# Kernel optimization log

Hardware: AMD Instinct MI355X
Metric: run time of the kernel (lower is better)

The kernel has to match this reference:

```python
import jax, jax.numpy as jnp
import numpy as np

E, B, S, C, N, D, DFF, H, K_FREQ = 4, 16, 256, 17, 16, 32, 64, 4, 4
DH = D // H
MA_KERNELS = (4, 8, 12)


def setup_inputs() -> dict:
    key = jax.random.key(0)
    ks = jax.random.split(key, 16)
    sc = 1.0 / np.sqrt(D).astype(np.float32)
    inp = {
        "x": jax.random.normal(ks[0], (B, S, C, 1), jnp.float32),
        "original_x": jax.random.uniform(ks[1], (B, S, 2), jnp.float32),
        "start_W": jax.random.normal(ks[2], (D,), jnp.float32),
        "start_b": jnp.zeros((D,), jnp.float32),
        "Wq": jax.random.normal(ks[3], (E, D, D), jnp.float32) * sc,
        "Wk": jax.random.normal(ks[4], (E, D, D), jnp.float32) * sc,
        "Wv": jax.random.normal(ks[5], (E, D, D), jnp.float32) * sc,
        "Wo": jax.random.normal(ks[6], (E, D, D), jnp.float32) * sc,
        "ln1_g": jnp.ones((E, D), jnp.float32),
        "ln1_b": jnp.zeros((E, D), jnp.float32),
        "ln2_g": jnp.ones((E, D), jnp.float32),
        "ln2_b": jnp.zeros((E, D), jnp.float32),
        "W1": jax.random.normal(ks[7], (E, D, DFF), jnp.float32) * sc,
        "b1": jnp.zeros((E, DFF), jnp.float32),
        "W2": jax.random.normal(ks[8], (E, DFF, D), jnp.float32) * (1.0 / np.sqrt(DFF).astype(np.float32)),
        "b2": jnp.zeros((E, D), jnp.float32),
    }
    return inp


def _moving_avg(x, k):
    # x: [B,S,Ch], replicate-pad then uniform window of size k (stride 1)
    front = jnp.repeat(x[:, :1], (k - 1) // 2, axis=1)
    end = jnp.repeat(x[:, -1:], k // 2, axis=1)
    xp = jnp.concatenate([front, x, end], axis=1)  # [B, S+k-1, Ch]
    c = jnp.cumsum(xp, axis=1)
    c = jnp.concatenate([jnp.zeros_like(c[:, :1]), c], axis=1)
    return (c[:, k:] - c[:, :-k]) / jnp.asarray(k, x.dtype)


def _fourier_season(x, k):
    # ETSformer-style FourierLayer: keep top-k amplitude frequencies (excluding DC)
    s = x.shape[1]
    xf = jnp.fft.rfft(x, axis=1)            # [B,F,Ch] complex
    amp = jnp.abs(xf)
    amp = amp.at[:, 0, :].set(-jnp.inf)     # exclude DC
    topv = jax.lax.top_k(jnp.moveaxis(amp, 1, -1), k)[0]  # [B,Ch,k]
    thresh = topv[..., -1]                  # [B,Ch]
    mask = amp >= thresh[:, None, :]
    xf_m = jnp.where(mask, xf, 0)
    return jnp.fft.irfft(xf_m, n=s, axis=1).astype(x.dtype)


def _ln(z, g, b):
    m = jnp.mean(z, -1, keepdims=True)
    v = jnp.var(z, -1, keepdims=True)
    return (z - m) * jax.lax.rsqrt(v + 1e-5) * g + b


def _expert_fwd(args):
    h, wq, wk, wv, wo, g1, bg1, g2, bg2, w1, b1e, w2, b2e = args
    # h: [B,S,N,D]; pre-LN MHA over the sequence axis per (batch, node)
    z = _ln(h, g1, bg1)
    q = jnp.einsum('bsnd,de->bsne', z, wq).reshape(B, S, N, H, DH)
    k_ = jnp.einsum('bsnd,de->bsne', z, wk).reshape(B, S, N, H, DH)
    v_ = jnp.einsum('bsnd,de->bsne', z, wv).reshape(B, S, N, H, DH)
    att = jnp.einsum('bqnhd,bknhd->bnhqk', q, k_) * (1.0 / np.sqrt(DH).astype(np.float32))
    att = jax.nn.softmax(att, axis=-1)
    o = jnp.einsum('bnhqk,bknhd->bqnhd', att, v_).reshape(B, S, N, D)
    h = h + jnp.einsum('bsnd,de->bsne', o, wo)
    z2 = _ln(h, g2, bg2)
    f = jax.nn.relu(jnp.einsum('bsnd,df->bsnf', z2, w1) + b1e)
    h = h + jnp.einsum('bsnf,fd->bsnd', f, w2) + b2e
    return h


def reference(x, original_x, start_W, start_b, Wq, Wk, Wv, Wo,
              ln1_g, ln1_b, ln2_g, ln2_b, W1, b1, W2, b2):
    xc = x[:, :, :, 0]                                  # [B,S,C]
    trend = sum(_moving_avg(xc, k) for k in MA_KERNELS) / float(len(MA_KERNELS))
    season = _fourier_season(xc, K_FREQ)
    new_x = xc + season + trend                         # [B,S,C]

    scores = original_x[:, :, -1]                       # [B,S]
    bins = jnp.linspace(scores.min(), scores.max(), E + 1)
    assign = jnp.clip(jnp.searchsorted(bins, scores, side='right') - 1, 0, E - 1)  # [B,S] int

    xns = new_x[:, :, :-1]                              # [B,S,N] drop score channel
    onehot = (assign[None] == jnp.arange(E)[:, None, None])          # [E,B,S] bool
    expert_in = xns[None] * onehot[..., None].astype(xns.dtype)      # [E,B,S,N] dense zero-padded dispatch
    hidden = expert_in[..., None] * start_W + start_b                # [E,B,S,N,D] start_linear

    outs = jax.lax.map(_expert_fwd, (hidden, Wq, Wk, Wv, Wo,
                                     ln1_g, ln1_b, ln2_g, ln2_b, W1, b1, W2, b2))  # [E,B,S,N,D]
    combined = jnp.einsum('ebs,ebsnd->bsnd', onehot.astype(outs.dtype), outs)      # one-hot combine
    return combined
```

## Files before the change

### kernel.cpp

```cpp
#include <hip/hip_runtime.h>
#include <math.h>

#define BB 16
#define SS 256
#define CC 17
#define NCH 16
#define DD 32
#define DFFN 64
#define HH 4
#define DH 8
#define EE 4

#define WS_K0 16
#define WS_V0 144
#define WS_XNS 512
#define WS_SPI (WS_XNS + BB*SS*NCH)
#define WS_WT  (WS_SPI + BB*SS + 64)
#define WS_WL  (WS_WT + 6144)

#define PRE 0.51006977f

typedef __fp16 hv2 __attribute__((ext_vector_type(2)));

__device__ __forceinline__ unsigned pkh2(float a, float b) {
  hv2 r = __builtin_amdgcn_cvt_pkrtz(a, b);
  unsigned u; __builtin_memcpy(&u, &r, 4);
  return u;
}
__device__ __forceinline__ float fd2(unsigned a, unsigned b, float c) {
  hv2 av, bv;
  __builtin_memcpy(&av, &a, 4);
  __builtin_memcpy(&bv, &b, 4);
  return __builtin_amdgcn_fdot2(av, bv, c, false);
}
__device__ __forceinline__ float h2lo(unsigned u) {
  hv2 v; __builtin_memcpy(&v, &u, 4); return (float)v[0];
}
__device__ __forceinline__ float h2hi(unsigned u) {
  hv2 v; __builtin_memcpy(&v, &u, 4); return (float)v[1];
}

__launch_bounds__(1024)
__global__ void decomp_prep_kernel(const float* __restrict__ x,
                                   const float* __restrict__ ox,
                                   const float* __restrict__ sb,
                                   const float* __restrict__ g1,
                                   const float* __restrict__ bb1,
                                   const float* __restrict__ Wq,
                                   const float* __restrict__ Wk,
                                   const float* __restrict__ Wv,
                                   const float* __restrict__ Wo,
                                   const float* __restrict__ W1,
                                   const float* __restrict__ W2,
                                   float* __restrict__ ws) {
  const int t = threadIdx.x;
  if (blockIdx.x < 256) {
    const int b = blockIdx.x / NCH;
    const int c = blockIdx.x % NCH;
    __shared__ float xs[SS];
    __shared__ float prr[1024], pii[1024];
    __shared__ float amp[129];
    __shared__ float2 YY[129];
    __shared__ float sth;
    if (t < SS) xs[t] = x[(b*SS + t)*CC + c];
    __syncthreads();
    const float TH0 = 0.024543692606170259f;
    {
      const int f = (t & 127) + 1;
      const int chunk = t >> 7;
      const int s0 = chunk * 32;
      const int ph0 = (f * s0) & 255;
      float si, cr; sincosf(TH0*(float)ph0, &si, &cr);
      float s1, c1; sincosf(TH0*(float)f, &s1, &c1);
      float xr = 0.f, xi = 0.f;
      #pragma unroll 4
      for (int k = 0; k < 32; ++k) {
        float xvv = xs[s0 + k];
        xr += xvv * cr;
        xi -= xvv * si;
        float nc = cr*c1 - si*s1;
        si = si*c1 + cr*s1;
        cr = nc;
      }
      prr[t] = xr; pii[t] = xi;
    }
    __syncthreads();
    if (t < 128) {
      float xr = 0.f, xi = 0.f;
      #pragma unroll
      for (int k2 = 0; k2 < 8; ++k2) { xr += prr[t + 128*k2]; xi += pii[t + 128*k2]; }
      prr[t] = xr; pii[t] = xi;
      amp[t+1] = sqrtf(xr*xr + xi*xi);
    }
    __syncthreads();
    if (t < 64) {
      float a0 = amp[t+1], a1 = amp[t+65];
      int i0 = t+1, i1 = t+65;
      float th = -1e30f;
      for (int r = 0; r < 4; ++r) {
        float mv = (a0 > a1) ? a0 : a1;
        int   mi = (a0 > a1) ? i0 : i1;
        for (int off = 32; off > 0; off >>= 1) {
          float ov = __shfl_xor(mv, off);
          int   oi = __shfl_xor(mi, off);
          if (ov > mv || (ov == mv && oi < mi)) { mv = ov; mi = oi; }
        }
        th = mv;
        if (mi == i0) a0 = -1e30f;
        if (mi == i1) a1 = -1e30f;
      }
      if (t == 0) sth = th;
    }
    __syncthreads();
    if (t < 128) {
      const int f = t + 1;
      float wgt = (amp[f] >= sth) ? ((f == 128) ? 1.0f : 2.0f) * (1.0f/256.0f) : 0.0f;
      YY[f] = make_float2(wgt * prr[t], wgt * pii[t]);
    }
    __syncthreads();
    {
      const int s = t & 255;
      const int fc = t >> 8;
      const int f0 = 1 + fc*32;
      const int ph0 = (s * f0) & 255;
      float si, cr; sincosf(TH0*(float)ph0, &si, &cr);
      float s1, c1; sincosf(TH0*(float)s, &s1, &c1);
      float acc = 0.f;
      #pragma unroll 4
      for (int k = 0; k < 32; ++k) {
        float2 y = YY[f0 + k];
        acc += y.x*cr - y.y*si;
        float nc = cr*c1 - si*s1;
        si = si*c1 + cr*s1;
        cr = nc;
      }
      prr[t] = acc;
    }
    __syncthreads();
    if (t < 256) {
      float season = prr[t] + prr[t+256] + prr[t+512] + prr[t+768];
      float s4 = 0.f, s8 = 0.f, s12 = 0.f;
      #pragma unroll
      for (int j = 0; j < 4; ++j)  { int p = t + j - 1; p = p < 0 ? 0 : (p > SS-1 ? SS-1 : p); s4  += xs[p]; }
      #pragma unroll
      for (int j = 0; j < 8; ++j)  { int p = t + j - 3; p = p < 0 ? 0 : (p > SS-1 ? SS-1 : p); s8  += xs[p]; }
      #pragma unroll
      for (int j = 0; j < 12; ++j) { int p = t + j - 5; p = p < 0 ? 0 : (p > SS-1 ? SS-1 : p); s12 += xs[p]; }
      float trend = (s4 * 0.25f + s8 * 0.125f + s12 * (1.0f/12.0f)) * (1.0f/3.0f);
      ws[WS_XNS + (b*SS + t)*NCH + c] = xs[t] + season + trend;
    }
  } else if (blockIdx.x < 272) {
    const int b = blockIdx.x - 256;
    __shared__ float red[32];
    __shared__ int asg[SS];
    __shared__ int cnt[EE];
    __shared__ float z0[EE*DD];
    float mn = 3e38f, mx = -3e38f;
    #pragma unroll
    for (int k = 0; k < 4; ++k) {
      float v = ox[(t + k*1024)*2 + 1];
      mn = fminf(mn, v); mx = fmaxf(mx, v);
    }
    for (int off = 32; off > 0; off >>= 1) {
      mn = fminf(mn, __shfl_xor(mn, off));
      mx = fmaxf(mx, __shfl_xor(mx, off));
    }
    if ((t & 63) == 0) { red[(t>>6)*2] = mn; red[(t>>6)*2+1] = mx; }
    __syncthreads();
    mn = red[0]; mx = red[1];
    #pragma unroll
    for (int w = 1; w < 16; ++w) { mn = fminf(mn, red[w*2]); mx = fmaxf(mx, red[w*2+1]); }
    const float step = (mx - mn) * 0.25f;
    const float e1 = mn + step, e2 = mn + 2.f*step, e3 = mn + 3.f*step;
    if (t < 256) {
      float sc = ox[(b*SS + t)*2 + 1];
      asg[t] = (sc >= e1) + (sc >= e2) + (sc >= e3);
    }
    __syncthreads();
    if (t < EE) {
      int c = 0;
      for (int s2 = 0; s2 < SS; ++s2) c += (asg[s2] == t);
      cnt[t] = c;
    }
    __syncthreads();
    int* SPw  = (int*)ws + WS_SPI;
    int* OFFw = SPw + BB*SS;
    if (t < EE) {
      int off = 0;
      for (int i = 0; i < t; ++i) off += cnt[i];
      OFFw[b*EE + t] = off;
      int kp = off;
      for (int s2 = 0; s2 < SS; ++s2) if (asg[s2] == t) SPw[b*SS + (kp++)] = s2;
    }
    if (t < 128) {
      int ee = t >> 5, d = t & 31;
      float m = 0.f;
      for (int i = 0; i < DD; ++i) m += sb[i];
      m *= (1.0f/DD);
      float var = 0.f;
      for (int i = 0; i < DD; ++i) { float df = sb[i]-m; var += df*df; }
      var *= (1.0f/DD);
      float rs = rsqrtf(var + 1e-5f);
      z0[ee*DD + d] = (sb[d]-m)*rs*g1[ee*DD+d] + bb1[ee*DD+d];
    }
    __syncthreads();
    if (b == 0 && t < 128) {
      int ee = t >> 5, d = t & 31;
      float k0 = 0.f, v0 = 0.f;
      for (int i = 0; i < DD; ++i) {
        float zz = z0[ee*DD + i];
        k0 += zz * Wk[ee*DD*DD + i*DD + d];
        v0 += zz * Wv[ee*DD*DD + i*DD + d];
      }
      ws[WS_K0 + ee*DD + d] = k0;
      ws[WS_V0 + ee*DD + d] = v0;
    }
  } else {
    unsigned* img = (unsigned*)ws + WS_WT;
    const int base_u = (blockIdx.x - 272)*4096;
    #pragma unroll
    for (int i = 0; i < 4; ++i) {
      int u = base_u + i*1024 + t;
      unsigned val;
      if (u < 6144) {
        int mat = u >> 11, r = u & 2047;
        int row = r >> 4, ip = r & 15;
        int e = row >> 5, q = row & 31;
        int d = (q & 3)*8 + (q >> 2);
        const float* Wm = (mat == 0) ? Wq : (mat == 1) ? Wk : Wv;
        const float* src = Wm + e*1024 + d;
        val = pkh2(src[ip*64], src[ip*64 + 32]);
      } else {
        int v = u - 6144;
        if (v < 2048) {
          int row = v >> 4, ip = v & 15;
          int e = row >> 5, q = row & 31;
          int d = (q & 3)*8 + (q >> 2);
          const float* src = Wo + e*1024 + d;
          val = pkh2(src[ip*64], src[ip*64 + 32]);
        } else if (v < 6144) {
          int r = v - 2048;
          int row = r >> 4, ip = r & 15;
          int e = row >> 6, q = row & 63;
          int j = (q & 3)*16 + (q >> 2);
          const float* src = W1 + e*2048 + j;
          val = pkh2(src[ip*128], src[ip*128 + 64]);
        } else {
          int r = v - 6144;
          int a = r >> 11, rr = r & 2047;
          int row = rr >> 4, ip = rr & 15;
          int e = row >> 5, q = row & 31;
          int d = (q & 3)*8 + (q >> 2);
          int jp = a*16 + ip;
          const float* src = W2 + e*2048 + d;
          val = pkh2(src[2*jp*32], src[(2*jp+1)*32]);
        }
      }
      img[u] = val;
    }
  }
}

__launch_bounds__(1024, 4)
__global__ void fused_kernel(const float* __restrict__ ws,
    const float* __restrict__ g1, const float* __restrict__ bb1,
    const float* __restrict__ sW, const float* __restrict__ sb,
    const float* __restrict__ g2, const float* __restrict__ bb2,
    const float* __restrict__ b1, const float* __restrict__ b2,
    float* __restrict__ out) {
  const int blk = blockIdx.x;
  const int n = blk & 15;
  const int b = blk >> 4;
  const int t = threadIdx.x;
  const int p = t >> 2;
  const int hh = t & 3;
  __shared__ unsigned lds[24576];
  float* fl = (float*)lds;
  unsigned* wT = lds + 8192;
  unsigned* wl = lds + 14336;

  {
    const uint4* simg = (const uint4*)((const unsigned*)ws + WS_WT);
    uint4* dst = (uint4*)wT;
    #pragma unroll
    for (int i = 0; i < 4; ++i) dst[i*1024 + t] = simg[i*1024 + t];
  }

  const int* SP  = (const int*)ws + WS_SPI;
  const int* OFF = SP + BB*SS;
  const int o1 = OFF[b*4+1], o2 = OFF[b*4+2], o3 = OFF[b*4+3];
  const int e = (p >= o1) + (p >= o2) + (p >= o3);
  const int beg = (e==0) ? 0  : ((e==1) ? o1 : ((e==2) ? o2 : o3));
  const int end = (e==0) ? o1 : ((e==1) ? o2 : ((e==2) ? o3 : SS));
  const int s = SP[b*SS + p];
  const float xv = ws[WS_XNS + (b*SS + s)*NCH + n];

  float h[DD];
  #pragma unroll
  for (int d = 0; d < DD; ++d) h[d] = xv * sW[d] + sb[d];
  float m = 0.f;
  #pragma unroll
  for (int d = 0; d < DD; ++d) m += h[d];
  m *= (1.0f/DD);
  float var = 0.f;
  #pragma unroll
  for (int d = 0; d < DD; ++d) { float df = h[d]-m; var += df*df; }
  var *= (1.0f/DD);
  float rs = rsqrtf(var + 1e-5f);
  unsigned zp[16];
  #pragma unroll
  for (int ip = 0; ip < 16; ++ip) {
    float za = (h[2*ip]  -m)*rs*g1[e*DD+2*ip]   + bb1[e*DD+2*ip];
    float zb = (h[2*ip+1]-m)*rs*g1[e*DD+2*ip+1] + bb1[e*DD+2*ip+1];
    zp[ip] = pkh2(za, zb);
  }
  __syncthreads();

  float q[DH], kk[DH], vv[DH];
  #pragma unroll
  for (int dd = 0; dd < DH; ++dd) {
    const int row16 = (e*32 + dd*4 + hh)*16;
    const uint4* rq = (const uint4*)&wT[row16];
    const uint4* rk = (const uint4*)&wT[2048 + row16];
    const uint4* rv = (const uint4*)&wT[4096 + row16];
    float aq = 0.f, ak = 0.f, av = 0.f;
    #pragma unroll
    for (int g4 = 0; g4 < 4; ++g4) {
      uint4 wq4 = rq[g4], wk4 = rk[g4], wv4 = rv[g4];
      aq = fd2(zp[4*g4+0], wq4.x, aq); aq = fd2(zp[4*g4+1], wq4.y, aq);
      aq = fd2(zp[4*g4+2], wq4.z, aq); aq = fd2(zp[4*g4+3], wq4.w, aq);
      ak = fd2(zp[4*g4+0], wk4.x, ak); ak = fd2(zp[4*g4+1], wk4.y, ak);
      ak = fd2(zp[4*g4+2], wk4.z, ak); ak = fd2(zp[4*g4+3], wk4.w, ak);
      av = fd2(zp[4*g4+0], wv4.x, av); av = fd2(zp[4*g4+1], wv4.y, av);
      av = fd2(zp[4*g4+2], wv4.z, av); av = fd2(zp[4*g4+3], wv4.w, av);
    }
    q[dd] = aq * PRE; kk[dd] = ak; vv[dd] = av;
  }
  *(uint4*)&lds[p*32 + hh*8]     = make_uint4(pkh2(kk[0],kk[1]), pkh2(kk[2],kk[3]),
                                              pkh2(kk[4],kk[5]), pkh2(kk[6],kk[7]));
  *(uint4*)&lds[p*32 + hh*8 + 4] = make_uint4(pkh2(vv[0],vv[1]), pkh2(vv[2],vv[3]),
                                              pkh2(vv[4],vv[5]), pkh2(vv[6],vv[7]));
  unsigned qp2[4];
  #pragma unroll
  for (int i = 0; i < 4; ++i) qp2[i] = pkh2(q[2*i], q[2*i+1]);
  float s0 = 0.f;
  #pragma unroll
  for (int d = 0; d < DH; ++d) s0 += q[d] * ws[WS_K0 + e*DD + hh*DH + d];
  float v0s[DH];
  #pragma unroll
  for (int d = 0; d < DH; ++d) v0s[d] = ws[WS_V0 + e*DD + hh*DH + d];
  __syncthreads();

  float wsum = 0.f;
  float o[DH] = {0,0,0,0,0,0,0,0};
  for (int jk = beg; jk < end; ++jk) {
    uint4 ku = *(const uint4*)&lds[jk*32 + hh*8];
    uint4 vu = *(const uint4*)&lds[jk*32 + hh*8 + 4];
    float a = 0.f;
    a = fd2(qp2[0], ku.x, a); a = fd2(qp2[1], ku.y, a);
    a = fd2(qp2[2], ku.z, a); a = fd2(qp2[3], ku.w, a);
    float w = __builtin_amdgcn_exp2f(a);
    wsum += w;
    o[0] += w*h2lo(vu.x); o[1] += w*h2hi(vu.x);
    o[2] += w*h2lo(vu.y); o[3] += w*h2hi(vu.y);
    o[4] += w*h2lo(vu.z); o[5] += w*h2hi(vu.z);
    o[6] += w*h2lo(vu.w); o[7] += w*h2hi(vu.w);
  }
  const int nmis = SS - (end - beg);
  float w0 = (float)nmis * __builtin_amdgcn_exp2f(s0);
  wsum += w0;
  #pragma unroll
  for (int d = 0; d < DH; ++d) o[d] += w0 * v0s[d];
  float inv = 1.0f / wsum;
  #pragma unroll
  for (int d = 0; d < DH; ++d) o[d] *= inv;
  __syncthreads();

  #pragma unroll
  for (int d = 0; d < DH; ++d) fl[p*33 + hh*DH + d] = o[d];
  __syncthreads();
  unsigned ovp[16];
  #pragma unroll
  for (int ip = 0; ip < 16; ++ip) ovp[ip] = pkh2(fl[p*33 + 2*ip], fl[p*33 + 2*ip+1]);

  float acc[DH];
  #pragma unroll
  for (int dd = 0; dd < DH; ++dd) {
    int d = hh*DH + dd;
    const uint4* row = (const uint4*)&wl[(e*32 + dd*4 + hh)*16];
    float a = xv * sW[d] + sb[d];
    #pragma unroll
    for (int g4 = 0; g4 < 4; ++g4) {
      uint4 w4 = row[g4];
      a = fd2(ovp[4*g4+0], w4.x, a); a = fd2(ovp[4*g4+1], w4.y, a);
      a = fd2(ovp[4*g4+2], w4.z, a); a = fd2(ovp[4*g4+3], w4.w, a);
    }
    acc[dd] = a;
  }
  __syncthreads();
  #pragma unroll
  for (int dd = 0; dd < DH; ++dd) fl[p*33 + hh*DH + dd] = acc[dd];
  __syncthreads();

  float h2r[DD];
  #pragma unroll
  for (int i = 0; i < DD; ++i) h2r[i] = fl[p*33 + i];
  m = 0.f;
  #pragma unroll
  for (int d = 0; d < DD; ++d) m += h2r[d];
  m *= (1.0f/DD);
  var = 0.f;
  #pragma unroll
  for (int d = 0; d < DD; ++d) { float df = h2r[d]-m; var += df*df; }
  var *= (1.0f/DD);
  rs = rsqrtf(var + 1e-5f);
  unsigned zp2[16];
  #pragma unroll
  for (int ip = 0; ip < 16; ++ip) {
    float za = (h2r[2*ip]  -m)*rs*g2[e*DD+2*ip]   + bb2[e*DD+2*ip];
    float zb = (h2r[2*ip+1]-m)*rs*g2[e*DD+2*ip+1] + bb2[e*DD+2*ip+1];
    zp2[ip] = pkh2(za, zb);
  }
  float hres[DH];
  #pragma unroll
  for (int dd = 0; dd < DH; ++dd) hres[dd] = h2r[hh*DH + dd];
  __syncthreads();

  float f[16];
  #pragma unroll
  for (int jj = 0; jj < 16; ++jj) {
    const uint4* row = (const uint4*)&wl[2048 + (e*64 + jj*4 + hh)*16];
    float a = b1[e*DFFN + hh*16 + jj];
    #pragma unroll
    for (int g4 = 0; g4 < 4; ++g4) {
      uint4 w4 = row[g4];
      a = fd2(zp2[4*g4+0], w4.x, a); a = fd2(zp2[4*g4+1], w4.y, a);
      a = fd2(zp2[4*g4+2], w4.z, a); a = fd2(zp2[4*g4+3], w4.w, a);
    }
    f[jj] = fmaxf(a, 0.0f);
  }
  {
    uint4 fa = make_uint4(pkh2(f[0],f[1]), pkh2(f[2],f[3]), pkh2(f[4],f[5]), pkh2(f[6],f[7]));
    uint4 fb = make_uint4(pkh2(f[8],f[9]), pkh2(f[10],f[11]), pkh2(f[12],f[13]), pkh2(f[14],f[15]));
    *(uint4*)&lds[p*36 + hh*8]     = fa;
    *(uint4*)&lds[p*36 + hh*8 + 4] = fb;
  }
  __syncthreads();

  uint4 fpr[8];
  #pragma unroll
  for (int g4 = 0; g4 < 8; ++g4) fpr[g4] = *(const uint4*)&lds[p*36 + 4*g4];
  float acc2[DH];
  #pragma unroll
  for (int dd = 0; dd < DH; ++dd) {
    int d = hh*DH + dd;
    const int row16 = (e*32 + dd*4 + hh)*16;
    float a = hres[dd] + b2[e*DD + d];
    #pragma unroll
    for (int g4 = 0; g4 < 8; ++g4) {
      const int plane = (g4 >> 2);
      uint4 w4 = *(const uint4*)&wl[6144 + plane*2048 + row16 + 4*(g4 & 3)];
      uint4 fq = fpr[g4];
      a = fd2(fq.x, w4.x, a); a = fd2(fq.y, w4.y, a);
      a = fd2(fq.z, w4.z, a); a = fd2(fq.w, w4.w, a);
    }
    acc2[dd] = a;
  }
  float* op = out + ((size_t)((b*SS + s)*NCH + n))*DD + hh*DH;
  *(float4*)(op)     = make_float4(acc2[0], acc2[1], acc2[2], acc2[3]);
  *(float4*)(op + 4) = make_float4(acc2[4], acc2[5], acc2[6], acc2[7]);
}

extern "C" void kernel_launch(void* const* d_in, const int* in_sizes, int n_in,
                              void* d_out, int out_size, void* d_ws, size_t ws_size,
                              hipStream_t stream) {
  (void)in_sizes; (void)n_in; (void)out_size; (void)ws_size;
  const float* x   = (const float*)d_in[0];
  const float* ox  = (const float*)d_in[1];
  const float* sW  = (const float*)d_in[2];
  const float* sb  = (const float*)d_in[3];
  const float* Wq  = (const float*)d_in[4];
  const float* Wk  = (const float*)d_in[5];
  const float* Wv  = (const float*)d_in[6];
  const float* Wo  = (const float*)d_in[7];
  const float* g1  = (const float*)d_in[8];
  const float* b1n = (const float*)d_in[9];
  const float* g2  = (const float*)d_in[10];
  const float* b2n = (const float*)d_in[11];
  const float* W1  = (const float*)d_in[12];
  const float* bf1 = (const float*)d_in[13];
  const float* W2  = (const float*)d_in[14];
  const float* bf2 = (const float*)d_in[15];
  float* out = (float*)d_out;
  float* ws  = (float*)d_ws;

  decomp_prep_kernel<<<276, 1024, 0, stream>>>(x, ox, sb, g1, b1n,
                                               Wq, Wk, Wv, Wo, W1, W2, ws);
  fused_kernel<<<BB*NCH, 1024, 0, stream>>>(ws, g1, b1n, sW, sb, g2, b2n,
                                            bf1, bf2, out);
}
```

Baseline: 145.6 us.

## Accumulate attention values in packed fp16, unroll key loop by two, async LDS weight load

The attention inner loop now keeps its value accumulator in packed half2 and uses hfma2 instead of eight scalar fp32 FMAs with unpacks. The loop is unrolled by two to add instruction-level parallelism. The weight image copy into LDS now uses global_load_lds direct transfers instead of going through registers. The fp16 accumulation of up to 256 terms risks precision loss. No explicit wait is added for the async LDS load beyond the existing barrier, which may be an ordering hazard.

```diff
diff --git a/kernel.cpp b/kernel.cpp
--- a/kernel.cpp
+++ b/kernel.cpp
@@ -1,4 +1,5 @@
 #include <hip/hip_runtime.h>
+#include <hip/hip_fp16.h>
 #include <math.h>
 
 #define BB 16
@@ -33,11 +34,8 @@
   __builtin_memcpy(&bv, &b, 4);
   return __builtin_amdgcn_fdot2(av, bv, c, false);
 }
-__device__ __forceinline__ float h2lo(unsigned u) {
-  hv2 v; __builtin_memcpy(&v, &u, 4); return (float)v[0];
-}
-__device__ __forceinline__ float h2hi(unsigned u) {
-  hv2 v; __builtin_memcpy(&v, &u, 4); return (float)v[1];
+__device__ __forceinline__ __half2 u2h2(unsigned u) {
+  __half2 h; __builtin_memcpy(&h, &u, 4); return h;
 }
 
 __launch_bounds__(1024)
@@ -280,18 +278,25 @@
   unsigned* wl = lds + 14336;
 
   {
-    const uint4* simg = (const uint4*)((const unsigned*)ws + WS_WT);
-    uint4* dst = (uint4*)wT;
-    #pragma unroll
-    for (int i = 0; i < 4; ++i) dst[i*1024 + t] = simg[i*1024 + t];
+    const unsigned* img = (const unsigned*)ws + WS_WT;
+    const int wv = t >> 6;
+    const int ln = t & 63;
+    #pragma unroll
+    for (int i = 0; i < 4; ++i) {
+      const int ch = wv*4 + i;
+      __builtin_amdgcn_global_load_lds(
+          (const __attribute__((address_space(1))) unsigned*)(img + ch*256 + ln*4),
+          (__attribute__((address_space(3))) unsigned*)(wT + ch*256 + ln*4),
+          16, 0, 0);
+    }
   }
 
   const int* SP  = (const int*)ws + WS_SPI;
   const int* OFF = SP + BB*SS;
-  const int o1 = OFF[b*4+1], o2 = OFF[b*4+2], o3 = OFF[b*4+3];
-  const int e = (p >= o1) + (p >= o2) + (p >= o3);
-  const int beg = (e==0) ? 0  : ((e==1) ? o1 : ((e==2) ? o2 : o3));
-  const int end = (e==0) ? o1 : ((e==1) ? o2 : ((e==2) ? o3 : SS));
+  const int o1 = OFF[b*4+1], o2v = OFF[b*4+2], o3 = OFF[b*4+3];
+  const int e = (p >= o1) + (p >= o2v) + (p >= o3);
+  const int beg = (e==0) ? 0  : ((e==1) ? o1 : ((e==2) ? o2v : o3));
+  const int end = (e==0) ? o1 : ((e==1) ? o2v : ((e==2) ? o3 : SS));
   const int s = SP[b*SS + p];
   const float xv = ws[WS_XNS + (b*SS + s)*NCH + n];
 
@@ -346,31 +351,62 @@
   float s0 = 0.f;
   #pragma unroll
   for (int d = 0; d < DH; ++d) s0 += q[d] * ws[WS_K0 + e*DD + hh*DH + d];
-  float v0s[DH];
-  #pragma unroll
-  for (int d = 0; d < DH; ++d) v0s[d] = ws[WS_V0 + e*DD + hh*DH + d];
   __syncthreads();
 
   float wsum = 0.f;
-  float o[DH] = {0,0,0,0,0,0,0,0};
-  for (int jk = beg; jk < end; ++jk) {
+  __half2 o2[4];
+  #pragma unroll
+  for (int i = 0; i < 4; ++i) o2[i] = u2h2(0u);
+  int jk = beg;
+  for (; jk + 1 < end; jk += 2) {
+    uint4 ku0 = *(const uint4*)&lds[jk*32 + hh*8];
+    uint4 vu0 = *(const uint4*)&lds[jk*32 + hh*8 + 4];
+    uint4 ku1 = *(const uint4*)&lds[(jk+1)*32 + hh*8];
+    uint4 vu1 = *(const uint4*)&lds[(jk+1)*32 + hh*8 + 4];
+    float a0 = 0.f, a1 = 0.f;
+    a0 = fd2(qp2[0], ku0.x, a0); a0 = fd2(qp2[1], ku0.y, a0);
+    a0 = fd2(qp2[2], ku0.z, a0); a0 = fd2(qp2[3], ku0.w, a0);
+    a1 = fd2(qp2[0], ku1.x, a1); a1 = fd2(qp2[1], ku1.y, a1);
+    a1 = fd2(qp2[2], ku1.z, a1); a1 = fd2(qp2[3], ku1.w, a1);
+    float w0f = __builtin_amdgcn_exp2f(a0);
+    float w1f = __builtin_amdgcn_exp2f(a1);
+    wsum += w0f + w1f;
+    __half2 w20 = u2h2(pkh2(w0f, w0f));
+    __half2 w21 = u2h2(pkh2(w1f, w1f));
+    o2[0] = __hfma2(w20, u2h2(vu0.x), o2[0]);
+    o2[1] = __hfma2(w20, u2h2(vu0.y), o2[1]);
+    o2[2] = __hfma2(w20, u2h2(vu0.z), o2[2]);
+    o2[3] = __hfma2(w20, u2h2(vu0.w), o2[3]);
+    o2[0] = __hfma2(w21, u2h2(vu1.x), o2[0]);
+    o2[1] = __hfma2(w21, u2h2(vu1.y), o2[1]);
+    o2[2] = __hfma2(w21, u2h2(vu1.z), o2[2]);
+    o2[3] = __hfma2(w21, u2h2(vu1.w), o2[3]);
+  }
+  if (jk < end) {
     uint4 ku = *(const uint4*)&lds[jk*32 + hh*8];
     uint4 vu = *(const uint4*)&lds[jk*32 + hh*8 + 4];
     float a = 0.f;
     a = fd2(qp2[0], ku.x, a); a = fd2(qp2[1], ku.y, a);
     a = fd2(qp2[2], ku.z, a); a = fd2(qp2[3], ku.w, a);
-    float w = __builtin_amdgcn_exp2f(a);
-    wsum += w;
-    o[0] += w*h2lo(vu.x); o[1] += w*h2hi(vu.x);
-    o[2] += w*h2lo(vu.y); o[3] += w*h2hi(vu.y);
-    o[4] += w*h2lo(vu.z); o[5] += w*h2hi(vu.z);
-    o[6] += w*h2lo(vu.w); o[7] += w*h2hi(vu.w);
+    float wf = __builtin_amdgcn_exp2f(a);
+    wsum += wf;
+    __half2 w2 = u2h2(pkh2(wf, wf));
+    o2[0] = __hfma2(w2, u2h2(vu.x), o2[0]);
+    o2[1] = __hfma2(w2, u2h2(vu.y), o2[1]);
+    o2[2] = __hfma2(w2, u2h2(vu.z), o2[2]);
+    o2[3] = __hfma2(w2, u2h2(vu.w), o2[3]);
+  }
+  float o[DH];
+  #pragma unroll
+  for (int i = 0; i < 4; ++i) {
+    o[2*i]   = __low2float(o2[i]);
+    o[2*i+1] = __high2float(o2[i]);
   }
   const int nmis = SS - (end - beg);
   float w0 = (float)nmis * __builtin_amdgcn_exp2f(s0);
   wsum += w0;
   #pragma unroll
-  for (int d = 0; d < DH; ++d) o[d] += w0 * v0s[d];
+  for (int d = 0; d < DH; ++d) o[d] += w0 * ws[WS_V0 + e*DD + hh*DH + d];
   float inv = 1.0f / wsum;
   #pragma unroll
   for (int d = 0; d < DH; ++d) o[d] *= inv;
```

Result: faster. 139.0 us (-4.5%).
